# Kernel tuning notes

Measured on AMD Instinct MI355X. Metric: run time of the kernel, lower is better.

## Reference

```python
import jax, jax.numpy as jnp
import numpy as np

DIM = 768
N_HEADS = 12
HEAD_DIM = DIM // N_HEADS
B, S = 16, 1024


def setup_inputs() -> dict:
    key = jax.random.key(0)
    k1, k2, k3, k4, k5 = jax.random.split(key, 5)
    scale = 0.02
    return {
        "x": jax.random.normal(k1, (B, S, DIM), dtype=jnp.float32),
        "W_attn": jax.random.normal(k2, (DIM, 3 * DIM), dtype=jnp.float32) * scale,
        "b_attn": jnp.zeros((3 * DIM,), dtype=jnp.float32),
        "W_proj": jax.random.normal(k3, (DIM, DIM), dtype=jnp.float32) * scale,
        "b_proj": jnp.zeros((DIM,), dtype=jnp.float32),
    }


def reference(x, W_attn, b_attn, W_proj, b_proj):
    # Dropout layers act as identity (eval mode) for a deterministic reference.
    Bsz, Sq, D = x.shape
    qkv = x @ W_attn + b_attn                      # [B, S, 3D]
    q, k, v = jnp.split(qkv, 3, axis=-1)
    q = q.reshape(Bsz, Sq, N_HEADS, HEAD_DIM)
    k = k.reshape(Bsz, Sq, N_HEADS, HEAD_DIM)
    v = v.reshape(Bsz, Sq, N_HEADS, HEAD_DIM)
    # scores: [B, H, S, S]
    w = jnp.einsum('bqhd,bkhd->bhqk', q, k) / jnp.sqrt(jnp.float32(HEAD_DIM))
    causal = jnp.tril(jnp.ones((Sq, Sq), dtype=bool))
    mask_value = jnp.finfo(w.dtype).min
    w = jnp.where(causal[None, None], w, mask_value)
    w = jax.nn.softmax(w, axis=-1)
    attn = jnp.einsum('bhqk,bkhd->bqhd', w, v).reshape(Bsz, Sq, D)
    return attn @ W_proj + b_proj
```

## Files before the change

kernel.cpp:

```cpp
#include <hip/hip_runtime.h>
#include <hip/hip_bf16.h>
#include <math.h>

#define BDIM 16
#define SEQ 1024
#define DIM 768
#define NH 12
#define HD 64
#define M_ROWS (BDIM * SEQ)
#define N_QKV (3 * DIM)
#define QN (BDIM * NH * SEQ * HD)

typedef __attribute__((ext_vector_type(8))) short bf16x8_t;
typedef __attribute__((ext_vector_type(4))) float f32x4_t;

__device__ __forceinline__ unsigned short f2bf(float x) {
    return __builtin_bit_cast(unsigned short, __float2bfloat16(x));
}

__device__ __forceinline__ void gld_lds16(const void* g, void* l) {
    __builtin_amdgcn_global_load_lds(
        (const __attribute__((address_space(1))) void*)g,
        (__attribute__((address_space(3))) void*)l, 16, 0, 0);
}

#define QSCALE 0.18033688011112042f

#define X_BLOCKS 6144
#define WA_TILES 432
#define WP_TILES 144

__global__ __launch_bounds__(256) void prep(
    const float* __restrict__ x, const float* __restrict__ Wa,
    const float* __restrict__ Wp,
    unsigned short* __restrict__ xb, unsigned short* __restrict__ Wat,
    unsigned short* __restrict__ Wpt)
{
    __shared__ unsigned short T[64][72];
    const int bid = blockIdx.x;
    const int tid = threadIdx.x;

    if (bid < X_BLOCKS) {
        size_t base = (size_t)bid * 2048 + tid * 8;
        float4 f0 = *(const float4*)&x[base];
        float4 f1 = *(const float4*)&x[base + 4];
        unsigned short tmp[8] = {f2bf(f0.x), f2bf(f0.y), f2bf(f0.z), f2bf(f0.w),
                                 f2bf(f1.x), f2bf(f1.y), f2bf(f1.z), f2bf(f1.w)};
        *(uint4*)&xb[base] = *(uint4*)tmp;
        return;
    }
    const float* W; unsigned short* Wt; int N, kt, nt;
    int b2 = bid - X_BLOCKS;
    if (b2 < WA_TILES) { W = Wa; Wt = Wat; N = N_QKV; kt = b2 / 36; nt = b2 % 36; }
    else { b2 -= WA_TILES; W = Wp; Wt = Wpt; N = DIM; kt = b2 / 12; nt = b2 % 12; }
    const int k0 = kt * 64, n0 = nt * 64;
#pragma unroll
    for (int c = 0; c < 4; c++) {
        int idx = c * 256 + tid;
        int r = idx >> 4;
        int c4 = (idx & 15) * 4;
        float4 v = *(const float4*)&W[(size_t)(k0 + r) * N + n0 + c4];
        T[r][c4 + 0] = f2bf(v.x);
        T[r][c4 + 1] = f2bf(v.y);
        T[r][c4 + 2] = f2bf(v.z);
        T[r][c4 + 3] = f2bf(v.w);
    }
    __syncthreads();
#pragma unroll
    for (int c = 0; c < 2; c++) {
        int idx = c * 256 + tid;
        int n = idx >> 3;
        int ch = (idx & 7) * 8;
        unsigned short tmp[8];
#pragma unroll
        for (int j = 0; j < 8; j++) tmp[j] = T[ch + j][n];
        *(uint4*)&Wt[(size_t)(n0 + n) * DIM + k0 + ch] = *(uint4*)tmp;
    }
}

__global__ __launch_bounds__(256) void gemm_qkv_mfma(
    const unsigned short* __restrict__ Ab,
    const unsigned short* __restrict__ Bt,
    const float* __restrict__ bias,
    unsigned short* __restrict__ Qo, unsigned short* __restrict__ Ko,
    unsigned short* __restrict__ Vt)
{
    __shared__ unsigned short smem[18432];
    unsigned short* As = smem;
    unsigned short* Bs = smem + 8192;

    const int tid = threadIdx.x;
    const int lane = tid & 63;
    const int w = tid >> 6;
    const int wm = w >> 1, wn = w & 1;
    const int ln = lane & 15, quad = lane >> 4;
    const int bm = blockIdx.y * 128, bn = blockIdx.x * 128;

    f32x4_t acc[4][4];
#pragma unroll
    for (int i = 0; i < 4; i++)
#pragma unroll
        for (int j = 0; j < 4; j++) acc[i][j] = (f32x4_t){0.f, 0.f, 0.f, 0.f};

    for (int k0 = 0; k0 < DIM; k0 += 64) {
        __syncthreads();
#pragma unroll
        for (int c = 0; c < 4; c++) {
            int idx = c * 256 + tid;
            int r = idx >> 3;
            int gch = (idx & 7) ^ (r & 7);
            gld_lds16(&Ab[(size_t)(bm + r) * DIM + k0 + gch * 8], &As[idx * 8]);
            gld_lds16(&Bt[(size_t)(bn + r) * DIM + k0 + gch * 8], &Bs[idx * 8]);
        }
        __syncthreads();

#pragma unroll
        for (int kk = 0; kk < 2; kk++) {
            bf16x8_t af[4], bfr[4];
#pragma unroll
            for (int mt = 0; mt < 4; mt++) {
                int r = wm * 64 + mt * 16 + ln;
                int c = (kk * 4 + quad) ^ (ln & 7);
                af[mt] = *(const bf16x8_t*)&As[r * 64 + c * 8];
            }
#pragma unroll
            for (int nt = 0; nt < 4; nt++) {
                int r = wn * 64 + nt * 16 + ln;
                int c = (kk * 4 + quad) ^ (ln & 7);
                bfr[nt] = *(const bf16x8_t*)&Bs[r * 64 + c * 8];
            }
#pragma unroll
            for (int mt = 0; mt < 4; mt++)
#pragma unroll
                for (int nt = 0; nt < 4; nt++)
                    acc[mt][nt] = __builtin_amdgcn_mfma_f32_16x16x32_bf16(
                        af[mt], bfr[nt], acc[mt][nt], 0, 0, 0);
        }
    }
    __syncthreads();

    const int nb = bn + wn * 64;
    const int part = nb / DIM;
    const int h = (nb % DIM) >> 6;
    const float scale = (part == 0) ? QSCALE : 1.0f;
    const int mb = bm + wm * 64;
    const int b_ = mb >> 10;
    const int s0 = mb & 1023;
    unsigned short* Wb = smem + w * 4608;

    float bias_v[4];
#pragma unroll
    for (int nt = 0; nt < 4; nt++) bias_v[nt] = bias[nb + nt * 16 + ln];

    if (part < 2) {
#pragma unroll
        for (int mt = 0; mt < 4; mt++)
#pragma unroll
            for (int nt = 0; nt < 4; nt++)
#pragma unroll
                for (int r = 0; r < 4; r++)
                    Wb[(mt * 16 + quad * 4 + r) * 72 + nt * 16 + ln] =
                        f2bf((acc[mt][nt][r] + bias_v[nt]) * scale);
        unsigned short* dst = (part == 0) ? Qo : Ko;
        size_t obase = (((size_t)b_ * NH + h) * SEQ + s0) * HD;
#pragma unroll
        for (int c = 0; c < 8; c++) {
            int idx = c * 64 + lane;
            int rr = idx >> 3;
            int ch = (idx & 7) * 8;
            *(uint4*)&dst[obase + (size_t)rr * HD + ch] = *(uint4*)&Wb[rr * 72 + ch];
        }
    } else {
#pragma unroll
        for (int mt = 0; mt < 4; mt++)
#pragma unroll
            for (int nt = 0; nt < 4; nt++)
#pragma unroll
                for (int r = 0; r < 4; r++)
                    Wb[(nt * 16 + ln) * 72 + mt * 16 + quad * 4 + r] =
                        f2bf(acc[mt][nt][r] + bias_v[nt]);
        size_t obase = ((size_t)b_ * NH + h) * (size_t)HD * SEQ;
#pragma unroll
        for (int c = 0; c < 8; c++) {
            int idx = c * 64 + lane;
            int d = idx >> 3;
            int ch = (idx & 7) * 8;
            *(uint4*)&Vt[obase + (size_t)d * SEQ + s0 + ch] = *(uint4*)&Wb[d * 72 + ch];
        }
    }
}

__global__ __launch_bounds__(256) void gemm_proj_mfma(
    const unsigned short* __restrict__ Ab,
    const unsigned short* __restrict__ Bt,
    const float* __restrict__ bias,
    float* __restrict__ C)
{
    __shared__ unsigned short smem[16384];
    unsigned short* As = smem;
    unsigned short* Bs = smem + 8192;

    const int tid = threadIdx.x;
    const int lane = tid & 63;
    const int w = tid >> 6;
    const int wm = w >> 1, wn = w & 1;
    const int ln = lane & 15, quad = lane >> 4;
    const int bm = blockIdx.y * 128, bn = blockIdx.x * 128;

    f32x4_t acc[4][4];
#pragma unroll
    for (int i = 0; i < 4; i++)
#pragma unroll
        for (int j = 0; j < 4; j++) acc[i][j] = (f32x4_t){0.f, 0.f, 0.f, 0.f};

    for (int k0 = 0; k0 < DIM; k0 += 64) {
        __syncthreads();
#pragma unroll
        for (int c = 0; c < 4; c++) {
            int idx = c * 256 + tid;
            int r = idx >> 3;
            int gch = (idx & 7) ^ (r & 7);
            gld_lds16(&Ab[(size_t)(bm + r) * DIM + k0 + gch * 8], &As[idx * 8]);
            gld_lds16(&Bt[(size_t)(bn + r) * DIM + k0 + gch * 8], &Bs[idx * 8]);
        }
        __syncthreads();

#pragma unroll
        for (int kk = 0; kk < 2; kk++) {
            bf16x8_t af[4], bfr[4];
#pragma unroll
            for (int mt = 0; mt < 4; mt++) {
                int r = wm * 64 + mt * 16 + ln;
                int c = (kk * 4 + quad) ^ (ln & 7);
                af[mt] = *(const bf16x8_t*)&As[r * 64 + c * 8];
            }
#pragma unroll
            for (int nt = 0; nt < 4; nt++) {
                int r = wn * 64 + nt * 16 + ln;
                int c = (kk * 4 + quad) ^ (ln & 7);
                bfr[nt] = *(const bf16x8_t*)&Bs[r * 64 + c * 8];
            }
#pragma unroll
            for (int mt = 0; mt < 4; mt++)
#pragma unroll
                for (int nt = 0; nt < 4; nt++)
                    acc[mt][nt] = __builtin_amdgcn_mfma_f32_16x16x32_bf16(
                        af[mt], bfr[nt], acc[mt][nt], 0, 0, 0);
        }
    }

    const int nb = bn + wn * 64;
    float bias_v[4];
#pragma unroll
    for (int nt = 0; nt < 4; nt++) bias_v[nt] = bias[nb + nt * 16 + ln];
#pragma unroll
    for (int mt = 0; mt < 4; mt++)
#pragma unroll
        for (int nt = 0; nt < 4; nt++)
#pragma unroll
            for (int r = 0; r < 4; r++) {
                int m = bm + wm * 64 + mt * 16 + quad * 4 + r;
                C[(size_t)m * DIM + nb + nt * 16 + ln] = acc[mt][nt][r] + bias_v[nt];
            }
}

__global__ __launch_bounds__(256, 3) void attn_mfma(
    const unsigned short* __restrict__ Qg, const unsigned short* __restrict__ Kg,
    const unsigned short* __restrict__ Vt, unsigned short* __restrict__ Out)
{
    __shared__ unsigned short Ks[2][4096];
    __shared__ unsigned short Vs[2][4096];
    __shared__ unsigned short Ps[4][2048];

    const int tid = threadIdx.x;
    const int lane = tid & 63;
    const int w = tid >> 6;
    const int ln = lane & 15;
    const int quad = lane >> 4;
    const int lnx = lane & 7;

    const int bh = blockIdx.y;
    const size_t gbase = (size_t)bh * SEQ * HD;
    const int b_ = bh / NH;
    const int h = bh % NH;

    const int srow = lane >> 3;
    const int scg = (lane & 7) ^ srow;

    for (int ph = 0; ph < 2; ph++) {
        const int qt = ph ? blockIdx.x : 7 - blockIdx.x;
        const int qbase = qt * 128;
        const int ntiles = 2 * qt + 2;

        bf16x8_t aq[2][2];
#pragma unroll
        for (int rg = 0; rg < 2; rg++)
#pragma unroll
            for (int p = 0; p < 2; p++)
                aq[rg][p] = *(const bf16x8_t*)
                    &Qg[gbase + (size_t)(qbase + w * 32 + rg * 16 + ln) * HD +
                        p * 32 + quad * 8];

        float l_r[2][4];
        f32x4_t acc_o[2][4];
#pragma unroll
        for (int rg = 0; rg < 2; rg++)
#pragma unroll
            for (int r = 0; r < 4; r++) {
                l_r[rg][r] = 0.f;
                acc_o[rg][r] = (f32x4_t){0.f, 0.f, 0.f, 0.f};
            }

        __syncthreads();

#pragma unroll
        for (int i = 0; i < 2; i++) {
            int s8 = w * 2 + i;
            int r = s8 * 8 + srow;
            gld_lds16(&Kg[gbase + (size_t)r * HD + scg * 8], &Ks[0][s8 * 512]);
            gld_lds16(&Vt[gbase + (size_t)r * SEQ + scg * 8], &Vs[0][s8 * 512]);
        }

        for (int t = 0; t < ntiles; t++) {
            const int k0 = t * 64;
            const int cur = t & 1;
            __syncthreads();

            if (t + 1 < ntiles) {
                const int nk0 = k0 + 64;
                const int nxt = cur ^ 1;
#pragma unroll
                for (int i = 0; i < 2; i++) {
                    int s8 = w * 2 + i;
                    int r = s8 * 8 + srow;
                    gld_lds16(&Kg[gbase + (size_t)(nk0 + r) * HD + scg * 8],
                              &Ks[nxt][s8 * 512]);
                    gld_lds16(&Vt[gbase + (size_t)r * SEQ + nk0 + scg * 8],
                              &Vs[nxt][s8 * 512]);
                }
            }

            f32x4_t s_acc[2][4];
#pragma unroll
            for (int ct = 0; ct < 4; ct++) {
                bf16x8_t bk0 = *(const bf16x8_t*)
                    &Ks[cur][(ct * 16 + ln) * 64 + ((0 + quad) ^ lnx) * 8];
                bf16x8_t bk1 = *(const bf16x8_t*)
                    &Ks[cur][(ct * 16 + ln) * 64 + ((4 + quad) ^ lnx) * 8];
#pragma unroll
                for (int rg = 0; rg < 2; rg++) {
                    f32x4_t s = (f32x4_t){0.f, 0.f, 0.f, 0.f};
                    s = __builtin_amdgcn_mfma_f32_16x16x32_bf16(aq[rg][0], bk0, s, 0, 0, 0);
                    s = __builtin_amdgcn_mfma_f32_16x16x32_bf16(aq[rg][1], bk1, s, 0, 0, 0);
                    s_acc[rg][ct] = s;
                }
            }

            const bool diag = (t >= 2 * qt);
#pragma unroll
            for (int rg = 0; rg < 2; rg++) {
                const int qrow = qbase + w * 32 + rg * 16 + quad * 4;
#pragma unroll
                for (int ct = 0; ct < 4; ct++) {
                    const int key = k0 + ct * 16 + ln;
#pragma unroll
                    for (int r = 0; r < 4; r++) {
                        float p = exp2f(s_acc[rg][ct][r]);
                        if (diag && key > qrow + r) p = 0.f;
                        s_acc[rg][ct][r] = p;
                        l_r[rg][r] += p;
                    }
                }
            }

#pragma unroll
            for (int rg = 0; rg < 2; rg++)
#pragma unroll
                for (int ct = 0; ct < 4; ct++)
#pragma unroll
                    for (int r = 0; r < 4; r++) {
                        int row = rg * 16 + quad * 4 + r;
                        int pc = (ct * 2 + (ln >> 3)) ^ (row & 7);
                        Ps[w][row * 64 + pc * 8 + lnx] = f2bf(s_acc[rg][ct][r]);
                    }

            bf16x8_t ap[2][2];
#pragma unroll
            for (int rg = 0; rg < 2; rg++)
#pragma unroll
                for (int p = 0; p < 2; p++)
                    ap[rg][p] = *(const bf16x8_t*)
                        &Ps[w][(rg * 16 + ln) * 64 + (((p * 4 + quad) ^ lnx)) * 8];

#pragma unroll
            for (int dt = 0; dt < 4; dt++) {
                bf16x8_t bv0 = *(const bf16x8_t*)
                    &Vs[cur][(dt * 16 + ln) * 64 + ((0 + quad) ^ lnx) * 8];
                bf16x8_t bv1 = *(const bf16x8_t*)
                    &Vs[cur][(dt * 16 + ln) * 64 + ((4 + quad) ^ lnx) * 8];
#pragma unroll
                for (int rg = 0; rg < 2; rg++) {
                    acc_o[rg][dt] = __builtin_amdgcn_mfma_f32_16x16x32_bf16(
                        ap[rg][0], bv0, acc_o[rg][dt], 0, 0, 0);
                    acc_o[rg][dt] = __builtin_amdgcn_mfma_f32_16x16x32_bf16(
                        ap[rg][1], bv1, acc_o[rg][dt], 0, 0, 0);
                }
            }
        }

#pragma unroll
        for (int off = 1; off < 16; off <<= 1)
#pragma unroll
            for (int rg = 0; rg < 2; rg++)
#pragma unroll
                for (int r = 0; r < 4; r++)
                    l_r[rg][r] += __shfl_xor(l_r[rg][r], off);

#pragma unroll
        for (int rg = 0; rg < 2; rg++) {
            float rinv[4];
#pragma unroll
            for (int r = 0; r < 4; r++) rinv[r] = 1.0f / l_r[rg][r];
#pragma unroll
            for (int dt = 0; dt < 4; dt++)
#pragma unroll
                for (int r = 0; r < 4; r++) {
                    int row = qbase + w * 32 + rg * 16 + quad * 4 + r;
                    Out[((size_t)b_ * SEQ + row) * DIM + h * HD + dt * 16 + ln] =
                        f2bf(acc_o[rg][dt][r] * rinv[r]);
                }
        }
    }
}

extern "C" void kernel_launch(void* const* d_in, const int* in_sizes, int n_in,
                              void* d_out, int out_size, void* d_ws, size_t ws_size,
                              hipStream_t stream) {
    const float* x  = (const float*)d_in[0];
    const float* Wa = (const float*)d_in[1];
    const float* ba = (const float*)d_in[2];
    const float* Wp = (const float*)d_in[3];
    const float* bp = (const float*)d_in[4];
    float* out = (float*)d_out;

    unsigned short* ws = (unsigned short*)d_ws;
    unsigned short* Qg  = ws;
    unsigned short* Kg  = Qg + (size_t)QN;
    unsigned short* Vt  = Kg + (size_t)QN;
    unsigned short* xb  = Vt + (size_t)QN;
    unsigned short* AO  = xb + (size_t)QN;
    unsigned short* Wat = AO + (size_t)QN;
    unsigned short* Wpt = Wat + (size_t)(N_QKV * DIM);

    prep<<<X_BLOCKS + WA_TILES + WP_TILES, 256, 0, stream>>>(
        x, Wa, Wp, xb, Wat, Wpt);

    dim3 g_qkv(N_QKV / 128, M_ROWS / 128);
    gemm_qkv_mfma<<<g_qkv, 256, 0, stream>>>(xb, Wat, ba, Qg, Kg, Vt);

    dim3 g_attn(4, BDIM * NH);
    attn_mfma<<<g_attn, 256, 0, stream>>>(Qg, Kg, Vt, AO);

    dim3 g_proj(DIM / 128, M_ROWS / 128);
    gemm_proj_mfma<<<g_proj, 256, 0, stream>>>(AO, Wpt, bp, out);
}
```

Measured before the change: 297.8 us.

## Double-buffer LDS tiles in QKV and projection GEMMs to overlap loads

```diff
diff --git a/kernel.cpp b/kernel.cpp
--- a/kernel.cpp
+++ b/kernel.cpp
@@ -78,16 +78,14 @@
     }
 }
 
-__global__ __launch_bounds__(256) void gemm_qkv_mfma(
+__global__ __launch_bounds__(256, 2) void gemm_qkv_mfma(
     const unsigned short* __restrict__ Ab,
     const unsigned short* __restrict__ Bt,
     const float* __restrict__ bias,
     unsigned short* __restrict__ Qo, unsigned short* __restrict__ Ko,
     unsigned short* __restrict__ Vt)
 {
-    __shared__ unsigned short smem[18432];
-    unsigned short* As = smem;
-    unsigned short* Bs = smem + 8192;
+    __shared__ unsigned short smem[32768];
 
     const int tid = threadIdx.x;
     const int lane = tid & 63;
@@ -102,17 +100,33 @@
 #pragma unroll
         for (int j = 0; j < 4; j++) acc[i][j] = (f32x4_t){0.f, 0.f, 0.f, 0.f};
 
-    for (int k0 = 0; k0 < DIM; k0 += 64) {
+#pragma unroll
+    for (int c = 0; c < 4; c++) {
+        int idx = c * 256 + tid;
+        int r = idx >> 3;
+        int gch = (idx & 7) ^ (r & 7);
+        gld_lds16(&Ab[(size_t)(bm + r) * DIM + gch * 8], &smem[idx * 8]);
+        gld_lds16(&Bt[(size_t)(bn + r) * DIM + gch * 8], &smem[8192 + idx * 8]);
+    }
+
+    for (int ki = 0; ki < 12; ki++) {
         __syncthreads();
-#pragma unroll
-        for (int c = 0; c < 4; c++) {
-            int idx = c * 256 + tid;
-            int r = idx >> 3;
-            int gch = (idx & 7) ^ (r & 7);
-            gld_lds16(&Ab[(size_t)(bm + r) * DIM + k0 + gch * 8], &As[idx * 8]);
-            gld_lds16(&Bt[(size_t)(bn + r) * DIM + k0 + gch * 8], &Bs[idx * 8]);
-        }
-        __syncthreads();
+        unsigned short* As = smem + (ki & 1) * 16384;
+        unsigned short* Bs = As + 8192;
+
+        if (ki < 11) {
+            const int nk0 = (ki + 1) * 64;
+            unsigned short* Asn = smem + ((ki + 1) & 1) * 16384;
+            unsigned short* Bsn = Asn + 8192;
+#pragma unroll
+            for (int c = 0; c < 4; c++) {
+                int idx = c * 256 + tid;
+                int r = idx >> 3;
+                int gch = (idx & 7) ^ (r & 7);
+                gld_lds16(&Ab[(size_t)(bm + r) * DIM + nk0 + gch * 8], &Asn[idx * 8]);
+                gld_lds16(&Bt[(size_t)(bn + r) * DIM + nk0 + gch * 8], &Bsn[idx * 8]);
+            }
+        }
 
 #pragma unroll
         for (int kk = 0; kk < 2; kk++) {
@@ -190,15 +204,13 @@
     }
 }
 
-__global__ __launch_bounds__(256) void gemm_proj_mfma(
+__global__ __launch_bounds__(256, 2) void gemm_proj_mfma(
     const unsigned short* __restrict__ Ab,
     const unsigned short* __restrict__ Bt,
     const float* __restrict__ bias,
     float* __restrict__ C)
 {
-    __shared__ unsigned short smem[16384];
-    unsigned short* As = smem;
-    unsigned short* Bs = smem + 8192;
+    __shared__ unsigned short smem[32768];
 
     const int tid = threadIdx.x;
     const int lane = tid & 63;
@@ -213,17 +225,33 @@
 #pragma unroll
         for (int j = 0; j < 4; j++) acc[i][j] = (f32x4_t){0.f, 0.f, 0.f, 0.f};
 
-    for (int k0 = 0; k0 < DIM; k0 += 64) {
+#pragma unroll
+    for (int c = 0; c < 4; c++) {
+        int idx = c * 256 + tid;
+        int r = idx >> 3;
+        int gch = (idx & 7) ^ (r & 7);
+        gld_lds16(&Ab[(size_t)(bm + r) * DIM + gch * 8], &smem[idx * 8]);
+        gld_lds16(&Bt[(size_t)(bn + r) * DIM + gch * 8], &smem[8192 + idx * 8]);
+    }
+
+    for (int ki = 0; ki < 12; ki++) {
         __syncthreads();
-#pragma unroll
-        for (int c = 0; c < 4; c++) {
-            int idx = c * 256 + tid;
-            int r = idx >> 3;
-            int gch = (idx & 7) ^ (r & 7);
-            gld_lds16(&Ab[(size_t)(bm + r) * DIM + k0 + gch * 8], &As[idx * 8]);
-            gld_lds16(&Bt[(size_t)(bn + r) * DIM + k0 + gch * 8], &Bs[idx * 8]);
-        }
-        __syncthreads();
+        unsigned short* As = smem + (ki & 1) * 16384;
+        unsigned short* Bs = As + 8192;
+
+        if (ki < 11) {
+            const int nk0 = (ki + 1) * 64;
+            unsigned short* Asn = smem + ((ki + 1) & 1) * 16384;
+            unsigned short* Bsn = Asn + 8192;
+#pragma unroll
+            for (int c = 0; c < 4; c++) {
+                int idx = c * 256 + tid;
+                int r = idx >> 3;
+                int gch = (idx & 7) ^ (r & 7);
+                gld_lds16(&Ab[(size_t)(bm + r) * DIM + nk0 + gch * 8], &Asn[idx * 8]);
+                gld_lds16(&Bt[(size_t)(bn + r) * DIM + nk0 + gch * 8], &Bsn[idx * 8]);
+            }
+        }
 
 #pragma unroll
         for (int kk = 0; kk < 2; kk++) {
```

Result: faster. 291.4 us (-2.1%).
